# Kernel tuning notes

Hardware: AMD Instinct MI355X
Metric: run time of the kernel (lower is better)

## Reference

```python
import jax, jax.numpy as jnp
import numpy as np

HEAD_SIZE = 256
N_EMBS = 1024
B, T = 8, 2048


def setup_inputs() -> dict:
    key = jax.random.key(0)
    kx, kq, kk, kv = jax.random.split(key, 4)
    # nn.Linear default init: U(-1/sqrt(fan_in), 1/sqrt(fan_in)); weights stored [out, in],
    # we store transposed [in, out] for x @ W.
    bound = 1.0 / np.sqrt(N_EMBS)
    x = jax.random.normal(kx, (B, T, N_EMBS), dtype=jnp.float32)
    Wq = jax.random.uniform(kq, (N_EMBS, HEAD_SIZE), dtype=jnp.float32, minval=-bound, maxval=bound)
    Wk = jax.random.uniform(kk, (N_EMBS, HEAD_SIZE), dtype=jnp.float32, minval=-bound, maxval=bound)
    Wv = jax.random.uniform(kv, (N_EMBS, HEAD_SIZE), dtype=jnp.float32, minval=-bound, maxval=bound)
    return {"x": x, "Wq": Wq, "Wk": Wk, "Wv": Wv}


def reference(x, Wq, Wk, Wv):
    # x: [B, T, C]
    Bn, Tn, C = x.shape
    Q = x @ Wq  # [B, T, H]
    K = x @ Wk
    V = x @ Wv
    scale = 1.0 / jnp.sqrt(jnp.asarray(HEAD_SIZE, dtype=x.dtype))
    w = jnp.einsum("bth,bsh->bts", Q, K) * scale  # [B, T, T]
    causal = jnp.tril(jnp.ones((Tn, Tn), dtype=bool))
    w = jnp.where(causal, w, -jnp.inf)
    w = jax.nn.softmax(w, axis=-1)
    out = jnp.einsum("bts,bsh->bth", w, V)  # [B, T, H]
    return out
```

## Files before the change

kernel.cpp:

```cpp
#include <hip/hip_runtime.h>

typedef short short8 __attribute__((ext_vector_type(8)));
typedef float floatx4 __attribute__((ext_vector_type(4)));

#define HEAD 256
#define CDIM 1024
#define TT   2048

#define WT_EL    0
#define QW_EL    786560
#define KW_EL    (QW_EL + 4194304)
#define VT_EL    (KW_EL + 4194304)
#define XC_EL    (VT_EL + 4194304)
#define NEED_FULL_BYTES ((size_t)(XC_EL + 16777216) * 2)

static __device__ __forceinline__ unsigned short f2bf(float f) {
    unsigned int u = __builtin_bit_cast(unsigned int, f);
    u += 0x7FFFu + ((u >> 16) & 1u);
    return (unsigned short)(u >> 16);
}
static __device__ __forceinline__ float bf2f(unsigned short h) {
    unsigned int u = ((unsigned int)h) << 16;
    return __builtin_bit_cast(float, u);
}

__device__ __forceinline__ void glds16(const void* g, void* l) {
    __builtin_amdgcn_global_load_lds(
        (const __attribute__((address_space(1))) void*)g,
        (__attribute__((address_space(3))) void*)l, 16, 0, 0);
}

__device__ __forceinline__ int probe_f32(const unsigned short* Wq, int flat_tid) {
    int lane = flat_tid & 63;
    int bad = 0;
    for (int i = lane; i < 512; i += 64)
        bad |= (((Wq[i] >> 7) & 0xFF) >= 128) ? 1 : 0;
#pragma unroll
    for (int off = 1; off < 64; off <<= 1) bad |= __shfl_xor(bad, off);
    return bad;
}

__global__ __launch_bounds__(256) void prep_kernel(
    const void* __restrict__ x, unsigned short* __restrict__ XT,
    const void* __restrict__ Wq, const void* __restrict__ Wk,
    const void* __restrict__ Wv, unsigned short* __restrict__ WtT) {
    __shared__ unsigned short tile[32][33];
    int t = threadIdx.x;
    int f = probe_f32((const unsigned short*)Wq, t);
    if (blockIdx.x < 8192) {
        int row = blockIdx.x * 2 + (t >> 7);
        int c8  = (t & 127) * 8;
        size_t si = (size_t)row * CDIM + c8;
        size_t di = (size_t)(row >> 7) * 131072 + (size_t)(c8 >> 6) * 8192
                  + (size_t)(row & 127) * 64 + (c8 & 63);
        short8 o;
        if (f) {
            const float* s = (const float*)x;
#pragma unroll
            for (int j = 0; j < 8; j++) o[j] = (short)f2bf(s[si + j]);
        } else {
            o = *(const short8*)((const unsigned short*)x + si);
        }
        *(short8*)&XT[di] = o;
    } else {
        int wid = blockIdx.x - 8192;
        int k0 = (wid & 31) * 32;
        int n0 = (wid >> 5) * 32;
        const void* W = (n0 < 256) ? Wq : (n0 < 512) ? Wk : Wv;
        int c0 = n0 & 255;
        int tx = t & 31, ty = t >> 5;
#pragma unroll
        for (int i = 0; i < 4; i++) {
            int r = ty + 8 * i;
            size_t idx = (size_t)(k0 + r) * HEAD + c0 + tx;
            tile[r][tx] = f ? f2bf(((const float*)W)[idx])
                            : ((const unsigned short*)W)[idx];
        }
        __syncthreads();
#pragma unroll
        for (int i = 0; i < 4; i++) {
            int n = n0 + ty + 8 * i;
            int k = k0 + tx;
            WtT[(size_t)(n >> 7) * 131072 + (size_t)(k >> 6) * 8192
                + (n & 127) * 64 + (k & 63)] = tile[tx][ty + 8 * i];
        }
    }
}

__global__ __launch_bounds__(256) void gemm_qkv(
    const unsigned short* __restrict__ XT,
    const unsigned short* __restrict__ WtT,
    unsigned short* __restrict__ Q,
    unsigned short* __restrict__ K,
    unsigned short* __restrict__ VT2) {
    __shared__ __attribute__((aligned(16))) short sh[16384];

    int tid  = threadIdx.x;
    int wave = tid >> 6, lane = tid & 63, quad = lane >> 4, lq = lane & 15;
    int wm = wave >> 1, wn = wave & 1;

    int id = blockIdx.x;
    int xcd = id & 7, g = id >> 3;
    int bn = g % 6;
    int bm = (g / 6) * 8 + xcd;
    int m0 = bm * 128, n0b = bn * 128;

    int l4 = lane >> 2;
    int cswz = ((lane & 3) ^ (l4 & 3) ^ ((l4 >> 2) & 3)) * 8;
    const unsigned short* gA = XT  + (size_t)bm * 131072
                               + (size_t)(wave * 32 + l4) * 64 + cswz;
    const unsigned short* gB = WtT + (size_t)bn * 131072
                               + (size_t)(wave * 32 + l4) * 64 + cswz;
    int rdswz = ((quad ^ (lq & 3) ^ ((lq >> 2) & 3))) * 8;

    floatx4 acc[4][4];
#pragma unroll
    for (int i = 0; i < 4; i++)
#pragma unroll
        for (int j = 0; j < 4; j++)
#pragma unroll
            for (int r = 0; r < 4; r++) acc[i][j][r] = 0.f;

    {
        short* dA = sh + wave * 1024;
        short* dB = sh + 4096 + wave * 1024;
        glds16(gA, dA); glds16(gA + 1024, dA + 512);
        glds16(gB, dB); glds16(gB + 1024, dB + 512);
    }

    int cur = 0;
    for (int s = 0; s < 32; s++) {
        __syncthreads();
        if (s + 1 < 32) {
            size_t off = (size_t)((s + 1) >> 1) * 8192 + ((s + 1) & 1) * 32;
            short* dA = sh + (cur ^ 1) * 8192 + wave * 1024;
            short* dB = sh + (cur ^ 1) * 8192 + 4096 + wave * 1024;
            glds16(gA + off, dA); glds16(gA + off + 1024, dA + 512);
            glds16(gB + off, dB); glds16(gB + off + 1024, dB + 512);
        }
        short* As_ = sh + cur * 8192;
        short* Bs_ = As_ + 4096;
        short8 af[4], bfv[4];
#pragma unroll
        for (int i = 0; i < 4; i++)
            af[i] = *(short8*)&As_[(64 * wm + 16 * i + lq) * 32 + rdswz];
#pragma unroll
        for (int j = 0; j < 4; j++)
            bfv[j] = *(short8*)&Bs_[(64 * wn + 16 * j + lq) * 32 + rdswz];
#pragma unroll
        for (int i = 0; i < 4; i++)
#pragma unroll
            for (int j = 0; j < 4; j++)
                acc[i][j] = __builtin_amdgcn_mfma_f32_16x16x32_bf16(
                    af[i], bfv[j], acc[i][j], 0, 0, 0);
        cur ^= 1;
    }

    int sel = n0b >> 8;
    if (sel < 2) {
        unsigned short* outp = (sel == 0) ? Q : K;
        float scale = (sel == 0) ? 0.0625f : 1.0f;
        int cbase = n0b & 255;
#pragma unroll
        for (int i = 0; i < 4; i++)
#pragma unroll
            for (int j = 0; j < 4; j++)
#pragma unroll
                for (int r = 0; r < 4; r++) {
                    int rr = m0 + 64 * wm + 16 * i + quad * 4 + r;
                    int cc = cbase + 64 * wn + 16 * j + lq;
                    outp[(size_t)rr * HEAD + cc] = f2bf(acc[i][j][r] * scale);
                }
    } else {
        int cbase = n0b - 512;
        int batch = m0 >> 11;
        int t0 = m0 & 2047;
        unsigned short* Vb = VT2 + (size_t)batch * HEAD * TT;
#pragma unroll
        for (int h = 0; h < 2; h++) {
            __syncthreads();
            if (wn == h) {
#pragma unroll
                for (int i = 0; i < 4; i++)
#pragma unroll
                    for (int j = 0; j < 4; j++)
#pragma unroll
                        for (int r = 0; r < 4; r++) {
                            int cl = 16 * j + lq;
                            int ml = 64 * wm + 16 * i + quad * 4 + r;
                            sh[cl * 136 + ml] = (short)f2bf(acc[i][j][r]);
                        }
            }
            __syncthreads();
            int cl = tid >> 2;
            int d = cbase + 64 * h + cl;
#pragma unroll
            for (int g2 = 0; g2 < 4; g2++) {
                int ms = (tid & 3) * 8 + g2 * 32;
                short8 v = *(short8*)&sh[cl * 136 + ms];
                int st = (t0 + ms) >> 5;
                int sc = ms & 31;
                *(short8*)&Vb[(size_t)st * 8192 + d * 32 + sc] = v;
            }
        }
    }
}

__global__ __launch_bounds__(256, 3) void attn(
    const unsigned short* __restrict__ Q,
    const unsigned short* __restrict__ K,
    const unsigned short* __restrict__ VT2,
    float* __restrict__ out,
    unsigned short* __restrict__ pO, float* __restrict__ pL) {
    __shared__ __attribute__((aligned(16))) short Ks[32 * 264];
    __shared__ __attribute__((aligned(16))) short Vt[256 * 40];
    __shared__ __attribute__((aligned(16))) short Ps[64 * 40];

    int tid  = threadIdx.x;
    int wave = tid >> 6, lane = tid & 63, quad = lane >> 4, lq = lane & 15;
    int j = blockIdx.x;
    int b = blockIdx.y;

    int qt, ci, nch;
    if (pO == nullptr) { qt = j; ci = 0; nch = 1; }
    else if (j < 8)    { qt = j; ci = 0; nch = 1; }
    else if (j < 24)   { qt = 8 + ((j - 8) >> 1);   ci = (j - 8) & 1;   nch = 2; }
    else if (j < 48)   { qt = 16 + (j - 24) / 3;    ci = (j - 24) % 3;  nch = 3; }
    else               { qt = 24 + ((j - 48) >> 2); ci = (j - 48) & 3;  nch = 4; }

    int t_lo = ci * 16;
    int t_hi = min(t_lo + 16, 2 * qt + 2);
    if (pO == nullptr) { t_lo = 0; t_hi = 2 * qt + 2; }
    bool direct = (nch == 1);

    int q0 = qt * 64;
    size_t boff = (size_t)b * TT * HEAD;
    const unsigned short* Qb = Q + boff;
    const unsigned short* Kb = K + boff;
    const unsigned short* Vg = VT2 + boff;

    short8 qf[8];
    int qrow = q0 + 16 * wave + lq;
#pragma unroll
    for (int kk = 0; kk < 8; kk++)
        qf[kk] = *(const short8*)&Qb[(size_t)qrow * HEAD + kk * 32 + quad * 8];

    float l_part[4];
    floatx4 accO[16];
#pragma unroll
    for (int r = 0; r < 4; r++) l_part[r] = 0.f;
#pragma unroll
    for (int n = 0; n < 16; n++)
#pragma unroll
        for (int r = 0; r < 4; r++) accO[n][r] = 0.f;

    int kr = tid >> 5, kc8 = (tid & 31) * 8;
    int vd = tid >> 2, vc8 = (tid & 3) * 8;

    short8 kreg[4], vreg[4];

    {
        int s0 = t_lo * 32;
#pragma unroll
        for (int g = 0; g < 4; g++)
            kreg[g] = *(const short8*)&Kb[(size_t)(s0 + g * 8 + kr) * HEAD + kc8];
#pragma unroll
        for (int g = 0; g < 4; g++)
            vreg[g] = *(const short8*)&Vg[(size_t)t_lo * 8192 + g * 2048 + tid * 8];
#pragma unroll
        for (int g = 0; g < 4; g++)
            *(short8*)&Ks[(g * 8 + kr) * 264 + kc8] = kreg[g];
#pragma unroll
        for (int g = 0; g < 4; g++)
            *(short8*)&Vt[(g * 64 + vd) * 40 + vc8] = vreg[g];
    }

    for (int it = t_lo; it < t_hi; it++) {
        __syncthreads();

        if (it + 1 < t_hi) {
            int s1 = (it + 1) * 32;
#pragma unroll
            for (int g = 0; g < 4; g++)
                kreg[g] = *(const short8*)&Kb[(size_t)(s1 + g * 8 + kr) * HEAD + kc8];
#pragma unroll
            for (int g = 0; g < 4; g++)
                vreg[g] = *(const short8*)&Vg[(size_t)(it + 1) * 8192 + g * 2048 + tid * 8];
        }

        floatx4 accS[2];
#pragma unroll
        for (int n = 0; n < 2; n++)
#pragma unroll
            for (int r = 0; r < 4; r++) accS[n][r] = 0.f;
#pragma unroll
        for (int kk = 0; kk < 8; kk++) {
            short8 a = qf[kk];
#pragma unroll
            for (int n = 0; n < 2; n++) {
                short8 bk = *(short8*)&Ks[(16 * n + lq) * 264 + kk * 32 + quad * 8];
                accS[n] = __builtin_amdgcn_mfma_f32_16x16x32_bf16(a, bk, accS[n], 0, 0, 0);
            }
        }

        if (it >= 2 * qt) {
            int s0 = it * 32;
#pragma unroll
            for (int n = 0; n < 2; n++) {
                int sg = s0 + 16 * n + lq;
#pragma unroll
                for (int r = 0; r < 4; r++) {
                    int qg = q0 + 16 * wave + quad * 4 + r;
                    if (sg > qg) accS[n][r] = -1e30f;
                }
            }
        }

#pragma unroll
        for (int n = 0; n < 2; n++)
#pragma unroll
            for (int r = 0; r < 4; r++) {
                float pv = __expf(accS[n][r] - 8.0f);
                l_part[r] += pv;
                Ps[(16 * wave + quad * 4 + r) * 40 + 16 * n + lq] =
                    (short)f2bf(pv);
            }

        {
            short8 ap = *(short8*)&Ps[(16 * wave + lq) * 40 + quad * 8];
#pragma unroll
            for (int n = 0; n < 16; n++) {
                short8 bv = *(short8*)&Vt[(16 * n + lq) * 40 + quad * 8];
                accO[n] = __builtin_amdgcn_mfma_f32_16x16x32_bf16(ap, bv, accO[n], 0, 0, 0);
            }
        }

        __syncthreads();
        if (it + 1 < t_hi) {
#pragma unroll
            for (int g = 0; g < 4; g++)
                *(short8*)&Ks[(g * 8 + kr) * 264 + kc8] = kreg[g];
#pragma unroll
            for (int g = 0; g < 4; g++)
                *(short8*)&Vt[(g * 64 + vd) * 40 + vc8] = vreg[g];
        }
    }

#pragma unroll
    for (int r = 0; r < 4; r++)
#pragma unroll
        for (int off = 1; off < 16; off <<= 1)
            l_part[r] += __shfl_xor(l_part[r], off);

    if (direct) {
        float* ob = out + boff;
#pragma unroll
        for (int r = 0; r < 4; r++) {
            float inv = 1.0f / l_part[r];
            int rr = q0 + 16 * wave + quad * 4 + r;
#pragma unroll
            for (int n = 0; n < 16; n++)
                ob[(size_t)rr * HEAD + 16 * n + lq] = accO[n][r] * inv;
        }
    } else {
        int sidx = (b * 32 + qt) * 4 + ci;
        unsigned short* po = pO + (size_t)sidx * 16384;
#pragma unroll
        for (int r = 0; r < 4; r++) {
            int rl = 16 * wave + quad * 4 + r;
#pragma unroll
            for (int n = 0; n < 16; n++)
                po[rl * 256 + 16 * n + lq] = f2bf(accO[n][r]);
        }
        if (lq == 0) {
#pragma unroll
            for (int r = 0; r < 4; r++)
                pL[sidx * 64 + 16 * wave + quad * 4 + r] = l_part[r];
        }
    }
}

__global__ __launch_bounds__(256) void reduce_attn(
    const unsigned short* __restrict__ pO, const float* __restrict__ pL,
    float* __restrict__ out) {
    int b = blockIdx.y, qt = 8 + blockIdx.x;
    int nch = (qt < 16) ? 2 : (qt < 24) ? 3 : 4;
    int base = (b * 32 + qt) * 4;
    int tid = threadIdx.x;
    __shared__ float ls[64];
    if (tid < 64) {
        float s = 0.f;
        for (int c = 0; c < nch; c++) s += pL[(base + c) * 64 + tid];
        ls[tid] = s;
    }
    __syncthreads();
    float* ob = out + (size_t)b * TT * HEAD + (size_t)qt * 64 * HEAD;
    for (int i = tid; i < 2048; i += 256) {
        int row = i >> 5, c8 = (i & 31) * 8;
        float a[8];
#pragma unroll
        for (int k = 0; k < 8; k++) a[k] = 0.f;
        for (int c = 0; c < nch; c++) {
            short8 v = *(const short8*)&pO[(size_t)(base + c) * 16384 + row * 256 + c8];
#pragma unroll
            for (int k = 0; k < 8; k++)
                a[k] += bf2f((unsigned short)v[k]);
        }
        float inv = 1.0f / ls[row];
#pragma unroll
        for (int k = 0; k < 8; k++)
            ob[(size_t)row * HEAD + c8 + k] = a[k] * inv;
    }
}

extern "C" void kernel_launch(void* const* d_in, const int* in_sizes, int n_in,
                              void* d_out, int out_size, void* d_ws, size_t ws_size,
                              hipStream_t stream) {
    const void* x  = d_in[0];
    const void* Wq = d_in[1];
    const void* Wk = d_in[2];
    const void* Wv = d_in[3];
    unsigned short* ws = (unsigned short*)d_ws;

    unsigned short* WtT = ws + WT_EL;
    unsigned short* Qw  = ws + QW_EL;
    unsigned short* Kw  = ws + KW_EL;
    unsigned short* VT2 = ws + VT_EL;
    unsigned short* xc  = ws + XC_EL;
    float* outp = (float*)d_out;

    bool full = (ws_size >= NEED_FULL_BYTES);

    const unsigned short* Xp;
    if (full) {
        prep_kernel<<<8960, 256, 0, stream>>>(x, xc, Wq, Wk, Wv, WtT);
        Xp = xc;
    } else {
        prep_kernel<<<dim3(768), 256, 0, stream>>>(x, xc, Wq, Wk, Wv, WtT);
        Xp = (const unsigned short*)x;
    }

    gemm_qkv<<<768, 256, 0, stream>>>(Xp, WtT, Qw, Kw, VT2);

    if (full) {
        unsigned short* pO = xc;
        float* pL = (float*)(ws + WT_EL);
        attn<<<dim3(80, 8), 256, 0, stream>>>(Qw, Kw, VT2, outp, pO, pL);
        reduce_attn<<<dim3(24, 8), 256, 0, stream>>>(pO, pL, outp);
    } else {
        attn<<<dim3(32, 8), 256, 0, stream>>>(Qw, Kw, VT2, outp,
                                              (unsigned short*)nullptr,
                                              (float*)nullptr);
    }
}
```

Baseline: 213.1 us.

## Restructure attention into 2-wave blocks with async double-buffered K and rebalanced split

Blocks shrink to 128 threads, and each wave now handles 32 query rows (two Q fragments), so every K and V fragment read feeds two MFMAs. K tiles go straight from global memory to LDS with an XOR swizzle and are double-buffered. This removes the register staging and the second barrier per iteration. V is read directly from global memory instead of being copied into LDS. The split-K scheme is replaced by a formula-driven chunking over 102 blocks per batch, launched heaviest first, with the reduce kernel updated to match. The trade-offs are more global traffic for V through the caches and higher register pressure from the doubled accumulators.

After: 268.5 us. +26.0%, slower.

```diff
diff --git a/kernel.cpp b/kernel.cpp
--- a/kernel.cpp
+++ b/kernel.cpp
@@ -6,6 +6,8 @@
 #define HEAD 256
 #define CDIM 1024
 #define TT   2048
+
+#define NBLK 102
 
 #define WT_EL    0
 #define QW_EL    786560
@@ -206,31 +208,35 @@
     }
 }
 
-__global__ __launch_bounds__(256, 3) void attn(
+__global__ __launch_bounds__(128, 2) void attn(
     const unsigned short* __restrict__ Q,
     const unsigned short* __restrict__ K,
     const unsigned short* __restrict__ VT2,
     float* __restrict__ out,
     unsigned short* __restrict__ pO, float* __restrict__ pL) {
-    __shared__ __attribute__((aligned(16))) short Ks[32 * 264];
-    __shared__ __attribute__((aligned(16))) short Vt[256 * 40];
+    __shared__ __attribute__((aligned(16))) short Ks[2][8192];
     __shared__ __attribute__((aligned(16))) short Ps[64 * 40];
 
     int tid  = threadIdx.x;
     int wave = tid >> 6, lane = tid & 63, quad = lane >> 4, lq = lane & 15;
-    int j = blockIdx.x;
     int b = blockIdx.y;
 
-    int qt, ci, nch;
-    if (pO == nullptr) { qt = j; ci = 0; nch = 1; }
-    else if (j < 8)    { qt = j; ci = 0; nch = 1; }
-    else if (j < 24)   { qt = 8 + ((j - 8) >> 1);   ci = (j - 8) & 1;   nch = 2; }
-    else if (j < 48)   { qt = 16 + (j - 24) / 3;    ci = (j - 24) % 3;  nch = 3; }
-    else               { qt = 24 + ((j - 48) >> 2); ci = (j - 48) & 3;  nch = 4; }
-
-    int t_lo = ci * 16;
-    int t_hi = min(t_lo + 16, 2 * qt + 2);
-    if (pO == nullptr) { t_lo = 0; t_hi = 2 * qt + 2; }
+    int qt, ci = 0, nch = 1, acc = 0;
+    if (pO == nullptr) {
+        qt = blockIdx.x;
+    } else {
+        int jr = NBLK - 1 - blockIdx.x;
+        qt = 0;
+        for (;;) {
+            int n = (2 * qt + 13) / 12;
+            if (jr < acc + n) { ci = jr - acc; nch = n; break; }
+            acc += n; qt++;
+        }
+    }
+    int T = 2 * qt + 2;
+    int csz = (T + nch - 1) / nch;
+    int t_lo = ci * csz;
+    int t_hi = min(t_lo + csz, T);
     bool direct = (nch == 1);
 
     int q0 = qt * 64;
@@ -239,153 +245,153 @@
     const unsigned short* Kb = K + boff;
     const unsigned short* Vg = VT2 + boff;
 
-    short8 qf[8];
-    int qrow = q0 + 16 * wave + lq;
-#pragma unroll
-    for (int kk = 0; kk < 8; kk++)
-        qf[kk] = *(const short8*)&Qb[(size_t)qrow * HEAD + kk * 32 + quad * 8];
-
-    float l_part[4];
-    floatx4 accO[16];
-#pragma unroll
-    for (int r = 0; r < 4; r++) l_part[r] = 0.f;
-#pragma unroll
-    for (int n = 0; n < 16; n++)
-#pragma unroll
-        for (int r = 0; r < 4; r++) accO[n][r] = 0.f;
-
-    int kr = tid >> 5, kc8 = (tid & 31) * 8;
-    int vd = tid >> 2, vc8 = (tid & 3) * 8;
-
-    short8 kreg[4], vreg[4];
-
-    {
-        int s0 = t_lo * 32;
-#pragma unroll
-        for (int g = 0; g < 4; g++)
-            kreg[g] = *(const short8*)&Kb[(size_t)(s0 + g * 8 + kr) * HEAD + kc8];
-#pragma unroll
-        for (int g = 0; g < 4; g++)
-            vreg[g] = *(const short8*)&Vg[(size_t)t_lo * 8192 + g * 2048 + tid * 8];
-#pragma unroll
-        for (int g = 0; g < 4; g++)
-            *(short8*)&Ks[(g * 8 + kr) * 264 + kc8] = kreg[g];
-#pragma unroll
-        for (int g = 0; g < 4; g++)
-            *(short8*)&Vt[(g * 64 + vd) * 40 + vc8] = vreg[g];
-    }
-
+    short8 qf[2][8];
+#pragma unroll
+    for (int i = 0; i < 2; i++) {
+        int qrow = q0 + 32 * wave + 16 * i + lq;
+#pragma unroll
+        for (int kk = 0; kk < 8; kk++)
+            qf[i][kk] = *(const short8*)&Qb[(size_t)qrow * HEAD + kk * 32 + quad * 8];
+    }
+
+    float l_part[2][4];
+    floatx4 accO[2][16];
+#pragma unroll
+    for (int i = 0; i < 2; i++) {
+#pragma unroll
+        for (int r = 0; r < 4; r++) l_part[i][r] = 0.f;
+#pragma unroll
+        for (int n = 0; n < 16; n++)
+#pragma unroll
+            for (int r = 0; r < 4; r++) accO[i][n][r] = 0.f;
+    }
+
+    int khalf = lane >> 5, kc = lane & 31;
+
+#define STAGE_K(buf, st_) do {                                            \
+        const unsigned short* _src = Kb + (size_t)(st_) * 8192;           \
+        _Pragma("unroll")                                                 \
+        for (int jj = 0; jj < 8; jj++) {                                  \
+            int _row = wave * 16 + jj * 2 + khalf;                        \
+            glds16(_src + _row * 256 + ((kc ^ (_row & 7)) << 3),          \
+                   &Ks[buf][wave * 4096 + jj * 512]);                     \
+        }                                                                 \
+    } while (0)
+
+    STAGE_K(0, t_lo);
+    int cur = 0;
     for (int it = t_lo; it < t_hi; it++) {
         __syncthreads();
-
-        if (it + 1 < t_hi) {
-            int s1 = (it + 1) * 32;
-#pragma unroll
-            for (int g = 0; g < 4; g++)
-                kreg[g] = *(const short8*)&Kb[(size_t)(s1 + g * 8 + kr) * HEAD + kc8];
-#pragma unroll
-            for (int g = 0; g < 4; g++)
-                vreg[g] = *(const short8*)&Vg[(size_t)(it + 1) * 8192 + g * 2048 + tid * 8];
-        }
-
-        floatx4 accS[2];
-#pragma unroll
-        for (int n = 0; n < 2; n++)
-#pragma unroll
-            for (int r = 0; r < 4; r++) accS[n][r] = 0.f;
+        if (it + 1 < t_hi) STAGE_K(cur ^ 1, it + 1);
+
+        const short* Kt = Ks[cur];
+        floatx4 accS[2][2];
+#pragma unroll
+        for (int i = 0; i < 2; i++)
+#pragma unroll
+            for (int n = 0; n < 2; n++)
+#pragma unroll
+                for (int r = 0; r < 4; r++) accS[i][n][r] = 0.f;
+
 #pragma unroll
         for (int kk = 0; kk < 8; kk++) {
-            short8 a = qf[kk];
-#pragma unroll
-            for (int n = 0; n < 2; n++) {
-                short8 bk = *(short8*)&Ks[(16 * n + lq) * 264 + kk * 32 + quad * 8];
-                accS[n] = __builtin_amdgcn_mfma_f32_16x16x32_bf16(a, bk, accS[n], 0, 0, 0);
-            }
+            short8 bk[2];
+#pragma unroll
+            for (int n = 0; n < 2; n++)
+                bk[n] = *(const short8*)&Kt[(16 * n + lq) * 256
+                        + (((kk * 4 + quad) ^ (lq & 7)) << 3)];
+#pragma unroll
+            for (int i = 0; i < 2; i++)
+#pragma unroll
+                for (int n = 0; n < 2; n++)
+                    accS[i][n] = __builtin_amdgcn_mfma_f32_16x16x32_bf16(
+                        qf[i][kk], bk[n], accS[i][n], 0, 0, 0);
         }
 
         if (it >= 2 * qt) {
             int s0 = it * 32;
 #pragma unroll
-            for (int n = 0; n < 2; n++) {
-                int sg = s0 + 16 * n + lq;
+            for (int i = 0; i < 2; i++)
+#pragma unroll
+                for (int n = 0; n < 2; n++) {
+                    int sg = s0 + 16 * n + lq;
+#pragma unroll
+                    for (int r = 0; r < 4; r++) {
+                        int qg = q0 + 32 * wave + 16 * i + quad * 4 + r;
+                        if (sg > qg) accS[i][n][r] = -1e30f;
+                    }
+                }
+        }
+
+#pragma unroll
+        for (int i = 0; i < 2; i++)
+#pragma unroll
+            for (int n = 0; n < 2; n++)
 #pragma unroll
                 for (int r = 0; r < 4; r++) {
-                    int qg = q0 + 16 * wave + quad * 4 + r;
-                    if (sg > qg) accS[n][r] = -1e30f;
+                    float pv = __expf(accS[i][n][r] - 8.0f);
+                    l_part[i][r] += pv;
+                    Ps[(32 * wave + 16 * i + quad * 4 + r) * 40 + 16 * n + lq] =
+                        (short)f2bf(pv);
                 }
-            }
-        }
-
-#pragma unroll
-        for (int n = 0; n < 2; n++)
-#pragma unroll
-            for (int r = 0; r < 4; r++) {
-                float pv = __expf(accS[n][r] - 8.0f);
-                l_part[r] += pv;
-                Ps[(16 * wave + quad * 4 + r) * 40 + 16 * n + lq] =
-                    (short)f2bf(pv);
-            }
-
-        {
-            short8 ap = *(short8*)&Ps[(16 * wave + lq) * 40 + quad * 8];
-#pragma unroll
-            for (int n = 0; n < 16; n++) {
-                short8 bv = *(short8*)&Vt[(16 * n + lq) * 40 + quad * 8];
-                accO[n] = __builtin_amdgcn_mfma_f32_16x16x32_bf16(ap, bv, accO[n], 0, 0, 0);
-            }
-        }
-
-        __syncthreads();
-        if (it + 1 < t_hi) {
-#pragma unroll
-            for (int g = 0; g < 4; g++)
-                *(short8*)&Ks[(g * 8 + kr) * 264 + kc8] = kreg[g];
-#pragma unroll
-            for (int g = 0; g < 4; g++)
-                *(short8*)&Vt[(g * 64 + vd) * 40 + vc8] = vreg[g];
-        }
-    }
-
-#pragma unroll
-    for (int r = 0; r < 4; r++)
-#pragma unroll
-        for (int off = 1; off < 16; off <<= 1)
-            l_part[r] += __shfl_xor(l_part[r], off);
+
+        short8 ap0 = *(short8*)&Ps[(32 * wave + lq) * 40 + quad * 8];
+        short8 ap1 = *(short8*)&Ps[(32 * wave + 16 + lq) * 40 + quad * 8];
+        const unsigned short* Vt = Vg + (size_t)it * 8192;
+#pragma unroll
+        for (int n = 0; n < 16; n++) {
+            short8 bv = *(const short8*)&Vt[(16 * n + lq) * 32 + quad * 8];
+            accO[0][n] = __builtin_amdgcn_mfma_f32_16x16x32_bf16(ap0, bv, accO[0][n], 0, 0, 0);
+            accO[1][n] = __builtin_amdgcn_mfma_f32_16x16x32_bf16(ap1, bv, accO[1][n], 0, 0, 0);
+        }
+        cur ^= 1;
+    }
+#undef STAGE_K
+
+#pragma unroll
+    for (int i = 0; i < 2; i++)
+#pragma unroll
+        for (int r = 0; r < 4; r++)
+#pragma unroll
+            for (int off = 1; off < 16; off <<= 1)
+                l_part[i][r] += __shfl_xor(l_part[i][r], off);
 
     if (direct) {
         float* ob = out + boff;
 #pragma unroll
-        for (int r = 0; r < 4; r++) {
-            float inv = 1.0f / l_part[r];
-            int rr = q0 + 16 * wave + quad * 4 + r;
-#pragma unroll
-            for (int n = 0; n < 16; n++)
-                ob[(size_t)rr * HEAD + 16 * n + lq] = accO[n][r] * inv;
-        }
-    } else {
-        int sidx = (b * 32 + qt) * 4 + ci;
+        for (int i = 0; i < 2; i++)
+#pragma unroll
+            for (int r = 0; r < 4; r++) {
+                float inv = 1.0f / l_part[i][r];
+                int rr = q0 + 32 * wave + 16 * i + quad * 4 + r;
+#pragma unroll
+                for (int n = 0; n < 16; n++)
+                    ob[(size_t)rr * HEAD + 16 * n + lq] = accO[i][n][r] * inv;
+            }
+    } else {
+        int sidx = b * NBLK + acc + ci;
         unsigned short* po = pO + (size_t)sidx * 16384;
 #pragma unroll
-        for (int r = 0; r < 4; r++) {
-            int rl = 16 * wave + quad * 4 + r;
-#pragma unroll
-            for (int n = 0; n < 16; n++)
-                po[rl * 256 + 16 * n + lq] = f2bf(accO[n][r]);
-        }
-        if (lq == 0) {
-#pragma unroll
-            for (int r = 0; r < 4; r++)
-                pL[sidx * 64 + 16 * wave + quad * 4 + r] = l_part[r];
-        }
+        for (int i = 0; i < 2; i++)
+#pragma unroll
+            for (int r = 0; r < 4; r++) {
+                int rl = 32 * wave + 16 * i + quad * 4 + r;
+#pragma unroll
+                for (int n = 0; n < 16; n++)
+                    po[rl * 256 + 16 * n + lq] = f2bf(accO[i][n][r]);
+                if (lq == 0) pL[sidx * 64 + rl] = l_part[i][r];
+            }
     }
 }
 
 __global__ __launch_bounds__(256) void reduce_attn(
     const unsigned short* __restrict__ pO, const float* __restrict__ pL,
     float* __restrict__ out) {
-    int b = blockIdx.y, qt = 8 + blockIdx.x;
-    int nch = (qt < 16) ? 2 : (qt < 24) ? 3 : 4;
-    int base = (b * 32 + qt) * 4;
+    int b = blockIdx.y, qt = 6 + blockIdx.x;
+    int pre = 6;
+    for (int k = 6; k < qt; k++) pre += (2 * k + 13) / 12;
+    int nch = (2 * qt + 13) / 12;
+    int base = b * NBLK + pre;
     int tid = threadIdx.x;
     __shared__ float ls[64];
     if (tid < 64) {
@@ -445,10 +451,10 @@
     if (full) {
         unsigned short* pO = xc;
         float* pL = (float*)(ws + WT_EL);
-        attn<<<dim3(80, 8), 256, 0, stream>>>(Qw, Kw, VT2, outp, pO, pL);
-        reduce_attn<<<dim3(24, 8), 256, 0, stream>>>(pO, pL, outp);
-    } else {
-        attn<<<dim3(32, 8), 256, 0, stream>>>(Qw, Kw, VT2, outp,
+        attn<<<dim3(NBLK, 8), 128, 0, stream>>>(Qw, Kw, VT2, outp, pO, pL);
+        reduce_attn<<<dim3(26, 8), 256, 0, stream>>>(pO, pL, outp);
+    } else {
+        attn<<<dim3(32, 8), 128, 0, stream>>>(Qw, Kw, VT2, outp,
                                               (unsigned short*)nullptr,
                                               (float*)nullptr);
     }
```

## Rebalance causal attention split-K chunks, swizzle LDS, raise occupancy

Applied to the files above, without the earlier changes.

Replaces the fixed 1-4 chunk split per query tile with a finer schedule of about one chunk per five key tiles, 119 blocks per batch, launched heaviest-first with even chunk sizes. The reduce kernel is updated to match the new partial-buffer indexing. K and P shared-memory tiles drop their padding and use XOR swizzles to avoid bank conflicts while using less LDS. The launch bound goes from 3 to 4 blocks per CU, which lowers the register budget and risks spills given the large accumulator array.

After: 343.1 us. 60.9% more time.

```diff
diff --git a/kernel.cpp b/kernel.cpp
--- a/kernel.cpp
+++ b/kernel.cpp
@@ -6,6 +6,8 @@
 #define HEAD 256
 #define CDIM 1024
 #define TT   2048
+
+#define NBLK 119
 
 #define WT_EL    0
 #define QW_EL    786560
@@ -206,31 +208,40 @@
     }
 }
 
-__global__ __launch_bounds__(256, 3) void attn(
+__global__ __launch_bounds__(256, 4) void attn(
     const unsigned short* __restrict__ Q,
     const unsigned short* __restrict__ K,
     const unsigned short* __restrict__ VT2,
     float* __restrict__ out,
     unsigned short* __restrict__ pO, float* __restrict__ pL) {
-    __shared__ __attribute__((aligned(16))) short Ks[32 * 264];
+    __shared__ __attribute__((aligned(16))) short Ks[32 * 256];
     __shared__ __attribute__((aligned(16))) short Vt[256 * 40];
-    __shared__ __attribute__((aligned(16))) short Ps[64 * 40];
+    __shared__ __attribute__((aligned(16))) short Ps[64 * 32];
 
     int tid  = threadIdx.x;
     int wave = tid >> 6, lane = tid & 63, quad = lane >> 4, lq = lane & 15;
-    int j = blockIdx.x;
     int b = blockIdx.y;
 
-    int qt, ci, nch;
-    if (pO == nullptr) { qt = j; ci = 0; nch = 1; }
-    else if (j < 8)    { qt = j; ci = 0; nch = 1; }
-    else if (j < 24)   { qt = 8 + ((j - 8) >> 1);   ci = (j - 8) & 1;   nch = 2; }
-    else if (j < 48)   { qt = 16 + (j - 24) / 3;    ci = (j - 24) % 3;  nch = 3; }
-    else               { qt = 24 + ((j - 48) >> 2); ci = (j - 48) & 3;  nch = 4; }
-
-    int t_lo = ci * 16;
-    int t_hi = min(t_lo + 16, 2 * qt + 2);
-    if (pO == nullptr) { t_lo = 0; t_hi = 2 * qt + 2; }
+    int qt, ci = 0, nch = 1, acc = 0;
+    if (pO == nullptr) {
+        qt = blockIdx.x;
+    } else {
+        int jr = NBLK - 1 - blockIdx.x;
+        qt = 0;
+        for (;;) {
+            int n = (2 * qt + 11) / 10;
+            if (jr < acc + n) { ci = jr - acc; nch = n; break; }
+            acc += n; qt++;
+        }
+    }
+    int T = 2 * qt + 2;
+    int t_lo, t_hi;
+    if (pO == nullptr) { t_lo = 0; t_hi = T; }
+    else {
+        int cb = T / nch, rem = T % nch;
+        t_lo = ci * cb + min(ci, rem);
+        t_hi = t_lo + cb + (ci < rem ? 1 : 0);
+    }
     bool direct = (nch == 1);
 
     int q0 = qt * 64;
@@ -254,7 +265,7 @@
 #pragma unroll
         for (int r = 0; r < 4; r++) accO[n][r] = 0.f;
 
-    int kr = tid >> 5, kc8 = (tid & 31) * 8;
+    int kr = tid >> 5, kc = tid & 31;
     int vd = tid >> 2, vc8 = (tid & 3) * 8;
 
     short8 kreg[4], vreg[4];
@@ -263,13 +274,13 @@
         int s0 = t_lo * 32;
 #pragma unroll
         for (int g = 0; g < 4; g++)
-            kreg[g] = *(const short8*)&Kb[(size_t)(s0 + g * 8 + kr) * HEAD + kc8];
+            kreg[g] = *(const short8*)&Kb[(size_t)(s0 + g * 8 + kr) * HEAD + kc * 8];
 #pragma unroll
         for (int g = 0; g < 4; g++)
             vreg[g] = *(const short8*)&Vg[(size_t)t_lo * 8192 + g * 2048 + tid * 8];
 #pragma unroll
         for (int g = 0; g < 4; g++)
-            *(short8*)&Ks[(g * 8 + kr) * 264 + kc8] = kreg[g];
+            *(short8*)&Ks[(g * 8 + kr) * 256 + ((kc ^ kr) << 3)] = kreg[g];
 #pragma unroll
         for (int g = 0; g < 4; g++)
             *(short8*)&Vt[(g * 64 + vd) * 40 + vc8] = vreg[g];
@@ -282,7 +293,7 @@
             int s1 = (it + 1) * 32;
 #pragma unroll
             for (int g = 0; g < 4; g++)
-                kreg[g] = *(const short8*)&Kb[(size_t)(s1 + g * 8 + kr) * HEAD + kc8];
+                kreg[g] = *(const short8*)&Kb[(size_t)(s1 + g * 8 + kr) * HEAD + kc * 8];
 #pragma unroll
             for (int g = 0; g < 4; g++)
                 vreg[g] = *(const short8*)&Vg[(size_t)(it + 1) * 8192 + g * 2048 + tid * 8];
@@ -298,16 +309,17 @@
             short8 a = qf[kk];
 #pragma unroll
             for (int n = 0; n < 2; n++) {
-                short8 bk = *(short8*)&Ks[(16 * n + lq) * 264 + kk * 32 + quad * 8];
+                short8 bk = *(short8*)&Ks[(16 * n + lq) * 256
+                            + (((kk * 4 + quad) ^ (lq & 7)) << 3)];
                 accS[n] = __builtin_amdgcn_mfma_f32_16x16x32_bf16(a, bk, accS[n], 0, 0, 0);
             }
         }
 
         if (it >= 2 * qt) {
-            int s0 = it * 32;
+            int s0m = it * 32;
 #pragma unroll
             for (int n = 0; n < 2; n++) {
-                int sg = s0 + 16 * n + lq;
+                int sg = s0m + 16 * n + lq;
 #pragma unroll
                 for (int r = 0; r < 4; r++) {
                     int qg = q0 + 16 * wave + quad * 4 + r;
@@ -322,12 +334,14 @@
             for (int r = 0; r < 4; r++) {
                 float pv = __expf(accS[n][r] - 8.0f);
                 l_part[r] += pv;
-                Ps[(16 * wave + quad * 4 + r) * 40 + 16 * n + lq] =
+                Ps[(16 * wave + quad * 4 + r) * 32
+                   + (((2 * n + (lq >> 3)) ^ r) << 3) + (lq & 7)] =
                     (short)f2bf(pv);
             }
 
         {
-            short8 ap = *(short8*)&Ps[(16 * wave + lq) * 40 + quad * 8];
+            short8 ap = *(short8*)&Ps[(16 * wave + lq) * 32
+                        + ((quad ^ (lq & 3)) << 3)];
 #pragma unroll
             for (int n = 0; n < 16; n++) {
                 short8 bv = *(short8*)&Vt[(16 * n + lq) * 40 + quad * 8];
@@ -339,7 +353,7 @@
         if (it + 1 < t_hi) {
 #pragma unroll
             for (int g = 0; g < 4; g++)
-                *(short8*)&Ks[(g * 8 + kr) * 264 + kc8] = kreg[g];
+                *(short8*)&Ks[(g * 8 + kr) * 256 + ((kc ^ kr) << 3)] = kreg[g];
 #pragma unroll
             for (int g = 0; g < 4; g++)
                 *(short8*)&Vt[(g * 64 + vd) * 40 + vc8] = vreg[g];
@@ -363,7 +377,7 @@
                 ob[(size_t)rr * HEAD + 16 * n + lq] = accO[n][r] * inv;
         }
     } else {
-        int sidx = (b * 32 + qt) * 4 + ci;
+        int sidx = b * NBLK + acc + ci;
         unsigned short* po = pO + (size_t)sidx * 16384;
 #pragma unroll
         for (int r = 0; r < 4; r++) {
@@ -383,9 +397,11 @@
 __global__ __launch_bounds__(256) void reduce_attn(
     const unsigned short* __restrict__ pO, const float* __restrict__ pL,
     float* __restrict__ out) {
-    int b = blockIdx.y, qt = 8 + blockIdx.x;
-    int nch = (qt < 16) ? 2 : (qt < 24) ? 3 : 4;
-    int base = (b * 32 + qt) * 4;
+    int b = blockIdx.y, qt = 5 + blockIdx.x;
+    int pre = 5;
+    for (int k = 5; k < qt; k++) pre += (2 * k + 11) / 10;
+    int nch = (2 * qt + 11) / 10;
+    int base = b * NBLK + pre;
     int tid = threadIdx.x;
     __shared__ float ls[64];
     if (tid < 64) {
@@ -445,8 +461,8 @@
     if (full) {
         unsigned short* pO = xc;
         float* pL = (float*)(ws + WT_EL);
-        attn<<<dim3(80, 8), 256, 0, stream>>>(Qw, Kw, VT2, outp, pO, pL);
-        reduce_attn<<<dim3(24, 8), 256, 0, stream>>>(pO, pL, outp);
+        attn<<<dim3(NBLK, 8), 256, 0, stream>>>(Qw, Kw, VT2, outp, pO, pL);
+        reduce_attn<<<dim3(27, 8), 256, 0, stream>>>(pO, pL, outp);
     } else {
         attn<<<dim3(32, 8), 256, 0, stream>>>(Qw, Kw, VT2, outp,
                                               (unsigned short*)nullptr,
```
